# Kernel tuning notes

Measured on AMD Instinct MI355X. Metric: run time of the kernel, lower is better.

The kernel has to match this reference:

```python
import itertools
import jax, jax.numpy as jnp
import numpy as np

B, N, C, O = 8, 32, 64, 64
PERMS = list(itertools.permutations((1, 2, 3)))  # build_idx_3_permutations order


def _lin(k, fan_in, out, lead=()):
    # torch nn.Linear default init: U(-1/sqrt(fan_in), 1/sqrt(fan_in)) for W and b
    kw, kb = jax.random.split(k)
    bound = 1.0 / float(np.sqrt(fan_in))
    W = jax.random.uniform(kw, lead + (fan_in, out), minval=-bound, maxval=bound, dtype=jnp.float32)
    b = jax.random.uniform(kb, lead + (out,), minval=-bound, maxval=bound, dtype=jnp.float32)
    return W, b


def setup_inputs() -> dict:
    key = jax.random.key(0)
    ks = jax.random.split(key, 8)
    x = jax.random.normal(ks[0], (B, N, N, N, C), dtype=jnp.float32)
    W33, b33 = _lin(ks[1], 6 * C, O)            # three_to_three linear
    W22, b22 = _lin(ks[2], 12 * C, O, (3,))     # two_to_two (a2 cat transpose), 3 diagonal planes
    W12, b12 = _lin(ks[3], 10 * C, O, (3,))     # one_to_two
    W12t, b12t = _lin(ks[4], 10 * C, O, (3,))   # one_to_two_t
    W02, b02 = _lin(ks[5], 5 * C, O, (3,))      # zero_to_two
    W11, b11 = _lin(ks[6], 10 * C, O)           # one_to_one (in_node_channels = 0)
    W01, b01 = _lin(ks[7], 5 * C, O)            # zero_to_one
    return dict(x=x, W33=W33, b33=b33, W22=W22, b22=b22, W12=W12, b12=b12,
                W12t=W12t, b12t=b12t, W02=W02, b02=b02, W11=W11, b11=b11,
                W01=W01, b01=b01)


def _contractions(x):
    """All second/first/zeroth-order mean contractions of x: [B,n,n,n,C]."""
    s1, s2, s3 = x.mean(1), x.mean(2), x.mean(3)                      # [B,n,n,C]
    # diagonals arranged as [B, other_axis, diag_axis, C]
    d12 = jnp.moveaxis(jnp.diagonal(x, axis1=1, axis2=2), -1, 2)      # [B,n3,diag,C]
    d13 = jnp.moveaxis(jnp.diagonal(x, axis1=1, axis2=3), -1, 2)      # [B,n2,diag,C]
    d23 = jnp.moveaxis(jnp.diagonal(x, axis1=2, axis2=3), -1, 2)      # [B,n1,diag,C]
    a2 = jnp.concatenate([s1, s2, s3, d12, d13, d23], axis=-1)        # [B,n,n,6C]
    tdiag = jnp.moveaxis(jnp.diagonal(d23, axis1=1, axis2=2), -1, 1)  # [B,n,C] triple diagonal x[b,i,i,i]
    a1 = jnp.concatenate([
        x.mean((1, 2)), x.mean((1, 3)), x.mean((2, 3)),               # double sums
        d12.mean(1), d12.mean(2), d13.mean(1), d13.mean(2),           # diag sums
        d23.mean(1), d23.mean(2),
        tdiag], axis=-1)                                              # [B,n,10C]
    a0 = jnp.concatenate([
        x.mean((1, 2, 3)),                                            # triple sum
        d12.mean((1, 2)), d13.mean((1, 2)), d23.mean((1, 2)),         # diag-sum-sum
        tdiag.mean(1)], axis=-1)                                      # [B,5C]
    return a2, a1, a0


def reference(x, W33, b33, W22, b22, W12, b12, W12t, b12t, W02, b02, W11, b11, W01, b01):
    n = x.shape[1]
    a2, a1, a0 = _contractions(x)
    # third-order mix: concat all 6 spatial permutations, then linear 6C -> O
    allp = jnp.concatenate([jnp.transpose(x, (0,) + p + (4,)) for p in PERMS], axis=-1)
    T = allp @ W33 + b33                                              # [B,n,n,n,O]
    # second-order mixes for the 3 diagonal planes
    a2wt = jnp.concatenate([a2, jnp.swapaxes(a2, 1, 2)], axis=-1)     # [B,n,n,12C]
    slices = []
    for i in range(3):
        m = a2wt @ W22[i] + b22[i]
        m = m + (a1 @ W12[i] + b12[i])[:, :, None, :]
        m = m + (a1 @ W12t[i] + b12t[i])[:, None, :, :]
        m = m + (a0 @ W02[i] + b02[i])[:, None, None, :]
        slices.append(m)                                              # [B,n(other),n(diag),O]
    # first-order (core-diagonal) mix
    mdiag = a1 @ W11 + b11 + (a0 @ W01 + b01)[:, None, :]             # [B,n,O]
    # _expand_mix: accumulate slices onto diagonal planes of T (diagonal_free=False)
    idx = jnp.arange(n)
    # plane (1,2): T[b,d,d,t] += slices[0][b,t,d]
    T = T.at[:, idx, idx].add(jnp.swapaxes(slices[0], 1, 2))
    # plane (1,3): T[b,d,t,d] += slices[1][b,t,d]
    Tsw = jnp.swapaxes(T, 2, 3)
    Tsw = Tsw.at[:, idx, idx].add(jnp.swapaxes(slices[1], 1, 2))
    T = jnp.swapaxes(Tsw, 2, 3)
    # plane (2,3): T[b,t,d,d] += slices[2][b,t,d]
    T = T.at[:, :, idx, idx].add(slices[2])
    # triple diagonal: T[b,d,d,d] += mdiag[b,d]
    T = T.at[:, idx, idx, idx].add(mdiag)
    return T
```

## Files before the change

### kernel.cpp

```cpp
#include <hip/hip_runtime.h>

#define NBATCH 8
#define NN 32
#define NC 64
#define NO 64
#define C6 384
#define C10 640
#define C12 768
#define C5 320

typedef __attribute__((ext_vector_type(8))) short short8;
typedef __attribute__((ext_vector_type(4))) float float4v;

static constexpr int OFF_ABF = 0;
static constexpr int OFF_A1  = 1572864;
static constexpr int OFF_A0  = 1736704;
static constexpr int OFF_R1  = 1739264;
static constexpr int OFF_R1T = 1788416;
static constexpr int OFF_R0  = 1837568;
static constexpr int OFF_MD  = 1839104;
static constexpr int OFF_WB  = 1855488;
static constexpr int OFF_WB2 = 1867776;

__device__ __forceinline__ unsigned short f2bf(float f) {
    union { float f; unsigned u; } x{f};
    unsigned r = x.u + 0x7fffu + ((x.u >> 16) & 1u);
    return (unsigned short)(r >> 16);
}

__device__ __forceinline__ void store_bf4(unsigned short* p, float4v v) {
    ushort4 w;
    w.x = f2bf(v.x); w.y = f2bf(v.y); w.z = f2bf(v.z); w.w = f2bf(v.w);
    *(ushort4*)p = w;
}

__device__ __forceinline__ float4v bf4(const unsigned short* p) {
    ushort4 u = *(const ushort4*)(p);
    float4v r;
    r.x = __uint_as_float((unsigned)u.x << 16);
    r.y = __uint_as_float((unsigned)u.y << 16);
    r.z = __uint_as_float((unsigned)u.z << 16);
    r.w = __uint_as_float((unsigned)u.w << 16);
    return r;
}

__global__ __launch_bounds__(256) void k_prepw(const float* __restrict__ W33,
                                               const float* __restrict__ W22,
                                               float* __restrict__ ws) {
    int id = blockIdx.x * 256 + threadIdx.x;
    if (id < 3072) {
        int lane = id & 63;
        int ks = (id >> 6) % 12;
        int nt = (id >> 6) / 12;
        int n = nt * 16 + (lane & 15);
        int k0 = ks * 32 + (lane >> 4) * 8;
        unsigned short* dst = (unsigned short*)(ws + OFF_WB) +
                              (size_t)((nt * 12 + ks) * 64 + lane) * 8;
#pragma unroll
        for (int jj = 0; jj < 8; ++jj) dst[jj] = f2bf(W33[(k0 + jj) * 64 + n]);
    } else if (id < 21504) {
        int q = id - 3072;
        int lane = q & 63;
        int ks = (q >> 6) % 24;
        int r = (q >> 6) / 24;
        int nt = r & 3;
        int i = r >> 2;
        int n = nt * 16 + (lane & 15);
        int k0 = ks * 32 + (lane >> 4) * 8;
        const float* W = W22 + (size_t)i * C12 * NO;
        unsigned short* dst = (unsigned short*)(ws + OFF_WB2) +
                              (size_t)(((i * 4 + nt) * 24 + ks) * 64 + lane) * 8;
#pragma unroll
        for (int jj = 0; jj < 8; ++jj) dst[jj] = f2bf(W[(k0 + jj) * 64 + n]);
    }
}

__global__ __launch_bounds__(256) void k_contract2(const float* __restrict__ x,
                                                   float* __restrict__ ws) {
    int id = blockIdx.x * 256 + threadIdx.x;
    int c4 = id & 15;
    int v = (id >> 4) & 31;
    int u = (id >> 9) & 31;
    int b = id >> 14;
    int bc = c4 * 4;
    const float* xb = x + (size_t)b * 2097152;

    float4v s1 = {0.f, 0.f, 0.f, 0.f}, s2 = s1, s3 = s1;
    {
        const float* p = xb + u * 2048 + v * 64 + bc;
        for (int i = 0; i < 32; ++i) s1 += *(const float4v*)(p + i * 65536);
    }
    {
        const float* p = xb + u * 65536 + v * 64 + bc;
        for (int j = 0; j < 32; ++j) s2 += *(const float4v*)(p + j * 2048);
    }
    {
        const float* p = xb + u * 65536 + v * 2048 + bc;
        for (int k = 0; k < 32; ++k) s3 += *(const float4v*)(p + k * 64);
    }
    float4v d12 = *(const float4v*)(xb + v * 65536 + v * 2048 + u * 64 + bc);
    float4v d13 = *(const float4v*)(xb + v * 65536 + u * 2048 + v * 64 + bc);
    float4v d23 = *(const float4v*)(xb + u * 65536 + v * 2048 + v * 64 + bc);

    const float inv = 1.0f / 32.0f;
    unsigned short* a2 = (unsigned short*)(ws + OFF_ABF) +
                         (size_t)((b * 32 + u) * 32 + v) * C6 + bc;
    store_bf4(a2 + 0 * 64, s1 * inv);
    store_bf4(a2 + 1 * 64, s2 * inv);
    store_bf4(a2 + 2 * 64, s3 * inv);
    store_bf4(a2 + 3 * 64, d12);
    store_bf4(a2 + 4 * 64, d13);
    store_bf4(a2 + 5 * 64, d23);
}

__global__ __launch_bounds__(256) void k_contract1(const float* __restrict__ x,
                                                   float* __restrict__ ws) {
    int id = blockIdx.x * 256 + threadIdx.x;
    int c4 = id & 15;
    int t = (id >> 4) & 31;
    int b = id >> 9;
    int bc = c4 * 4;
    const unsigned short* a2 = (const unsigned short*)(ws + OFF_ABF) +
                               (size_t)b * 32 * 32 * C6;

    float4v su0 = {0.f,0.f,0.f,0.f}, su3 = su0, su4 = su0, su5 = su0;
    float4v sv0 = su0, sv1 = su0, sv3 = su0, sv4 = su0, sv5 = su0;
    for (int u = 0; u < 32; ++u) {
        const unsigned short* row = a2 + (size_t)(u * 32 + t) * C6 + bc;
        su0 += bf4(row + 0);
        su3 += bf4(row + 192);
        su4 += bf4(row + 256);
        su5 += bf4(row + 320);
    }
    for (int v = 0; v < 32; ++v) {
        const unsigned short* row = a2 + (size_t)(t * 32 + v) * C6 + bc;
        sv0 += bf4(row + 0);
        sv1 += bf4(row + 64);
        sv3 += bf4(row + 192);
        sv4 += bf4(row + 256);
        sv5 += bf4(row + 320);
    }
    float4v td = *(const float4v*)(x + (((size_t)b * 32 + t) * 32 + t) * 2048 + t * 64 + bc);

    float* a1 = ws + OFF_A1 + ((size_t)b * 32 + t) * C10;
    const float inv = 1.0f / 32.0f;
    *(float4v*)(a1 + 0 * 64 + bc) = su0 * inv;
    *(float4v*)(a1 + 1 * 64 + bc) = sv0 * inv;
    *(float4v*)(a1 + 2 * 64 + bc) = sv1 * inv;
    *(float4v*)(a1 + 3 * 64 + bc) = su3 * inv;
    *(float4v*)(a1 + 4 * 64 + bc) = sv3 * inv;
    *(float4v*)(a1 + 5 * 64 + bc) = su4 * inv;
    *(float4v*)(a1 + 6 * 64 + bc) = sv4 * inv;
    *(float4v*)(a1 + 7 * 64 + bc) = su5 * inv;
    *(float4v*)(a1 + 8 * 64 + bc) = sv5 * inv;
    *(float4v*)(a1 + 9 * 64 + bc) = td;
}

__global__ __launch_bounds__(256) void k_contract0(float* __restrict__ ws) {
    int id = blockIdx.x * 256 + threadIdx.x;
    if (id >= 512) return;
    int c = id & 63;
    int b = id >> 6;
    const float* a1 = ws + OFF_A1 + (size_t)b * 32 * C10;
    float s0 = 0, s1 = 0, s2 = 0, s3 = 0, s4 = 0;
    for (int t = 0; t < 32; ++t) {
        const float* row = a1 + t * C10;
        s0 += row[0 * 64 + c];
        s1 += row[3 * 64 + c];
        s2 += row[5 * 64 + c];
        s3 += row[7 * 64 + c];
        s4 += row[9 * 64 + c];
    }
    float* a0 = ws + OFF_A0 + b * C5;
    const float inv = 1.0f / 32.0f;
    a0[0 * 64 + c] = s0 * inv;
    a0[1 * 64 + c] = s1 * inv;
    a0[2 * 64 + c] = s2 * inv;
    a0[3 * 64 + c] = s3 * inv;
    a0[4 * 64 + c] = s4 * inv;
}

__global__ __launch_bounds__(256) void k_rowmix(
    const float* __restrict__ W12, const float* __restrict__ b12,
    const float* __restrict__ W12t, const float* __restrict__ b12t,
    const float* __restrict__ W02, const float* __restrict__ b02,
    const float* __restrict__ W11, const float* __restrict__ b11,
    const float* __restrict__ W01, const float* __restrict__ b01,
    float* __restrict__ ws) {
    int id = blockIdx.x * 256 + threadIdx.x;
    if (id < 98304) {
        bool second = id >= 49152;
        int q = second ? id - 49152 : id;
        int o = q & 63;
        int t = (q >> 6) & 31;
        int b = (q >> 11) & 7;
        int i = q >> 14;
        const float* W = (second ? W12t : W12) + (size_t)i * C10 * NO;
        const float* bb = (second ? b12t : b12) + i * NO;
        const float* a1 = ws + OFF_A1 + ((size_t)b * 32 + t) * C10;
        float acc = bb[o];
        for (int m = 0; m < C10; ++m) acc += a1[m] * W[m * NO + o];
        ws[(second ? OFF_R1T : OFF_R1) + (((size_t)i * 8 + b) * 32 + t) * NO + o] = acc;
    } else if (id < 114688) {
        int q = id - 98304;
        int o = q & 63;
        int t = (q >> 6) & 31;
        int b = q >> 11;
        const float* a1 = ws + OFF_A1 + ((size_t)b * 32 + t) * C10;
        const float* a0 = ws + OFF_A0 + (size_t)b * C5;
        float acc = b11[o] + b01[o];
        for (int m = 0; m < C10; ++m) acc += a1[m] * W11[m * NO + o];
        for (int m = 0; m < C5; ++m) acc += a0[m] * W01[m * NO + o];
        ws[OFF_MD + ((size_t)b * 32 + t) * NO + o] = acc;
    } else if (id < 116224) {
        int q = id - 114688;
        int o = q & 63;
        int b = (q >> 6) & 7;
        int i = q >> 9;
        const float* a0 = ws + OFF_A0 + (size_t)b * C5;
        float acc = b02[i * NO + o];
        for (int m = 0; m < C5; ++m) acc += a0[m] * W02[(size_t)i * C5 * NO + m * NO + o];
        ws[OFF_R0 + ((size_t)i * 8 + b) * NO + o] = acc;
    }
}

__global__ __launch_bounds__(256) void k_main(const float* __restrict__ x,
                                              const float* __restrict__ ws,
                                              const float* __restrict__ b33,
                                              float* __restrict__ T) {
    __shared__ __align__(16) unsigned short As[32 * 392];
    int tid = threadIdx.x;
    const unsigned short* WB = (const unsigned short*)(ws + OFF_WB);

    int wv = tid >> 6;
    int lane = tid & 63;
    int m_tile = wv & 1;
    int n_pair = wv >> 1;
    int colq = lane & 15;
    int quad = lane >> 4;

    short8 bfr[2][12];
#pragma unroll
    for (int np = 0; np < 2; ++np) {
        int nt = n_pair * 2 + np;
#pragma unroll
        for (int ks = 0; ks < 12; ++ks)
            bfr[np][ks] = *(const short8*)(WB + (size_t)((nt * 12 + ks) * 64 + lane) * 8);
    }
    float bb0 = b33[(n_pair * 2 + 0) * 16 + colq];
    float bb1 = b33[(n_pair * 2 + 1) * 16 + colq];

    int k0 = wv * 8;
    int c = colq * 4;
    int mrow = m_tile * 16 + colq;
    const unsigned short* Arow = &As[mrow * 392 + quad * 8];

    int tbase = (blockIdx.x & 7) * 1024 + (blockIdx.x >> 3) * 4;
#pragma unroll 1
    for (int r = 0; r < 4; ++r) {
        int tile = tbase + r;
        int b = tile >> 10;
        int i = (tile >> 5) & 31;
        int j = tile & 31;
        const float* xb = x + (size_t)b * 2097152;

#pragma unroll
        for (int half = 0; half < 2; ++half) {
            int k = k0 + quad + half * 4;
            float4v v0 = *(const float4v*)(xb + i * 65536 + j * 2048 + k * 64 + c);
            float4v v1 = *(const float4v*)(xb + i * 65536 + k * 2048 + j * 64 + c);
            float4v v2 = *(const float4v*)(xb + j * 65536 + i * 2048 + k * 64 + c);
            float4v v3 = *(const float4v*)(xb + k * 65536 + i * 2048 + j * 64 + c);
            float4v v4 = *(const float4v*)(xb + j * 65536 + k * 2048 + i * 64 + c);
            float4v v5 = *(const float4v*)(xb + k * 65536 + j * 2048 + i * 64 + c);
            unsigned short* dst = &As[k * 392 + c];
            store_bf4(dst + 0 * 64, v0);
            store_bf4(dst + 1 * 64, v1);
            store_bf4(dst + 2 * 64, v2);
            store_bf4(dst + 3 * 64, v3);
            store_bf4(dst + 4 * 64, v4);
            store_bf4(dst + 5 * 64, v5);
        }
        __syncthreads();

        float4v acc0 = {0.f, 0.f, 0.f, 0.f};
        float4v acc1 = {0.f, 0.f, 0.f, 0.f};
#pragma unroll
        for (int ks = 0; ks < 12; ++ks) {
            short8 a = *(const short8*)(Arow + ks * 32);
            acc0 = __builtin_amdgcn_mfma_f32_16x16x32_bf16(a, bfr[0][ks], acc0, 0, 0, 0);
            acc1 = __builtin_amdgcn_mfma_f32_16x16x32_bf16(a, bfr[1][ks], acc1, 0, 0, 0);
        }

        float* Tb = T + (size_t)tile * 2048;
#pragma unroll
        for (int rr = 0; rr < 4; ++rr) {
            int m = m_tile * 16 + quad * 4 + rr;
            int o0 = (n_pair * 2 + 0) * 16 + colq;
            int o1 = (n_pair * 2 + 1) * 16 + colq;
            __builtin_nontemporal_store(acc0[rr] + bb0, &Tb[m * 64 + o0]);
            __builtin_nontemporal_store(acc1[rr] + bb1, &Tb[m * 64 + o1]);
        }
        __syncthreads();
    }
}

__global__ __launch_bounds__(256) void k_slices(const float* __restrict__ b22,
                                                float* __restrict__ T,
                                                const float* __restrict__ ws) {
    __shared__ __align__(16) unsigned short As[32 * 776];
    int blk = blockIdx.x;
    int b = blk >> 5;
    int t = blk & 31;
    int tid = threadIdx.x;
    const unsigned short* abf = (const unsigned short*)(ws + OFF_ABF);
    const unsigned short* WB2 = (const unsigned short*)(ws + OFF_WB2);

    for (int l = tid; l < 3072; l += 256) {
        int d = l / 96;
        int m8 = l - d * 96;
        const unsigned short* src = (m8 < 48)
            ? abf + (size_t)(((b * 32 + t) * 32 + d) * C6) + m8 * 8
            : abf + (size_t)(((b * 32 + d) * 32 + t) * C6) + (m8 - 48) * 8;
        *(short8*)&As[d * 776 + m8 * 8] = *(const short8*)src;
    }
    __syncthreads();

    int wv = tid >> 6;
    int lane = tid & 63;
    int mt = wv & 1;
    int nh = wv >> 1;
    float4v zero = {0.f, 0.f, 0.f, 0.f};
    float4v acc[3][2] = {{zero, zero}, {zero, zero}, {zero, zero}};
    const unsigned short* Arow = &As[(mt * 16 + (lane & 15)) * 776 + (lane >> 4) * 8];
#pragma unroll
    for (int ks = 0; ks < 24; ++ks) {
        short8 a = *(const short8*)(Arow + ks * 32);
#pragma unroll
        for (int i = 0; i < 3; ++i) {
#pragma unroll
            for (int np = 0; np < 2; ++np) {
                int nt = nh * 2 + np;
                short8 bf = *(const short8*)(WB2 + (size_t)(((i * 4 + nt) * 24 + ks) * 64 + lane) * 8);
                acc[i][np] = __builtin_amdgcn_mfma_f32_16x16x32_bf16(a, bf, acc[i][np], 0, 0, 0);
            }
        }
    }

    int colq = lane & 15;
    int quad = lane >> 4;
    float* Tb = T + (size_t)b * 2097152;
#pragma unroll
    for (int np = 0; np < 2; ++np) {
        int o = (nh * 2 + np) * 16 + colq;
        float base0 = b22[0 * 64 + o] + ws[OFF_R1 + ((size_t)(0 * 8 + b) * 32 + t) * 64 + o]
                    + ws[OFF_R0 + (size_t)(0 * 8 + b) * 64 + o];
        float base1 = b22[1 * 64 + o] + ws[OFF_R1 + ((size_t)(1 * 8 + b) * 32 + t) * 64 + o]
                    + ws[OFF_R0 + (size_t)(1 * 8 + b) * 64 + o];
        float base2 = b22[2 * 64 + o] + ws[OFF_R1 + ((size_t)(2 * 8 + b) * 32 + t) * 64 + o]
                    + ws[OFF_R0 + (size_t)(2 * 8 + b) * 64 + o];
#pragma unroll
        for (int r = 0; r < 4; ++r) {
            int d = mt * 16 + quad * 4 + r;
            float s0 = acc[0][np][r] + base0 + ws[OFF_R1T + ((size_t)(0 * 8 + b) * 32 + d) * 64 + o];
            float s1 = acc[1][np][r] + base1 + ws[OFF_R1T + ((size_t)(1 * 8 + b) * 32 + d) * 64 + o];
            float s2 = acc[2][np][r] + base2 + ws[OFF_R1T + ((size_t)(2 * 8 + b) * 32 + d) * 64 + o];
            if (d != t) {
                Tb[d * 65536 + d * 2048 + t * 64 + o] += s0;
                Tb[d * 65536 + t * 2048 + d * 64 + o] += s1;
                Tb[t * 65536 + d * 2048 + d * 64 + o] += s2;
            } else {
                float md = ws[OFF_MD + ((size_t)b * 32 + d) * 64 + o];
                Tb[d * 65536 + d * 2048 + d * 64 + o] += s0 + s1 + s2 + md;
            }
        }
    }
}

extern "C" void kernel_launch(void* const* d_in, const int* in_sizes, int n_in,
                              void* d_out, int out_size, void* d_ws, size_t ws_size,
                              hipStream_t stream) {
    const float* x    = (const float*)d_in[0];
    const float* W33  = (const float*)d_in[1];
    const float* b33  = (const float*)d_in[2];
    const float* W22  = (const float*)d_in[3];
    const float* b22  = (const float*)d_in[4];
    const float* W12  = (const float*)d_in[5];
    const float* b12  = (const float*)d_in[6];
    const float* W12t = (const float*)d_in[7];
    const float* b12t = (const float*)d_in[8];
    const float* W02  = (const float*)d_in[9];
    const float* b02  = (const float*)d_in[10];
    const float* W11  = (const float*)d_in[11];
    const float* b11  = (const float*)d_in[12];
    const float* W01  = (const float*)d_in[13];
    const float* b01  = (const float*)d_in[14];
    float* T  = (float*)d_out;
    float* ws = (float*)d_ws;

    hipLaunchKernelGGL(k_prepw, dim3(84), dim3(256), 0, stream, W33, W22, ws);
    hipLaunchKernelGGL(k_contract2, dim3(512), dim3(256), 0, stream, x, ws);
    hipLaunchKernelGGL(k_contract1, dim3(16), dim3(256), 0, stream, x, ws);
    hipLaunchKernelGGL(k_contract0, dim3(2), dim3(256), 0, stream, ws);
    hipLaunchKernelGGL(k_rowmix, dim3(454), dim3(256), 0, stream,
                       W12, b12, W12t, b12t, W02, b02, W11, b11, W01, b01, ws);
    hipLaunchKernelGGL(k_main, dim3(2048), dim3(256), 0, stream, x, ws, b33, T);
    hipLaunchKernelGGL(k_slices, dim3(256), dim3(256), 0, stream, b22, T, ws);
}
```

Baseline: 277.0 us.

## Parallelize contract1 across blocks, fuse contract0 via atomics, widen k_slices

k_contract1 now runs one block per (batch, t) with a shared-memory tree reduction instead of 16 blocks of serial 32-step loops. The old k_contract0 kernel is folded in through atomicAdd into a0, which is zeroed with a memset beforehand. k_slices moves to 512 threads so each wave owns one N-tile instead of two, giving more waves per block. The goal is to remove tiny low-occupancy launches from the critical path. The cost is float atomics with nondeterministic summation order and an extra memset on the stream.

New measurement: 250.4 us. 9.6% less time.

```diff
diff --git a/kernel.cpp b/kernel.cpp
--- a/kernel.cpp
+++ b/kernel.cpp
@@ -115,69 +115,72 @@
 
 __global__ __launch_bounds__(256) void k_contract1(const float* __restrict__ x,
                                                    float* __restrict__ ws) {
-    int id = blockIdx.x * 256 + threadIdx.x;
-    int c4 = id & 15;
-    int t = (id >> 4) & 31;
-    int b = id >> 9;
+    __shared__ float4v red[16][148];
+    int blk = blockIdx.x;
+    int b = blk >> 5;
+    int t = blk & 31;
+    int tid = threadIdx.x;
+    int c4 = tid & 15;
+    int q = tid >> 4;
     int bc = c4 * 4;
     const unsigned short* a2 = (const unsigned short*)(ws + OFF_ABF) +
                                (size_t)b * 32 * 32 * C6;
 
-    float4v su0 = {0.f,0.f,0.f,0.f}, su3 = su0, su4 = su0, su5 = su0;
-    float4v sv0 = su0, sv1 = su0, sv3 = su0, sv4 = su0, sv5 = su0;
-    for (int u = 0; u < 32; ++u) {
-        const unsigned short* row = a2 + (size_t)(u * 32 + t) * C6 + bc;
-        su0 += bf4(row + 0);
-        su3 += bf4(row + 192);
-        su4 += bf4(row + 256);
-        su5 += bf4(row + 320);
-    }
-    for (int v = 0; v < 32; ++v) {
-        const unsigned short* row = a2 + (size_t)(t * 32 + v) * C6 + bc;
-        sv0 += bf4(row + 0);
-        sv1 += bf4(row + 64);
-        sv3 += bf4(row + 192);
-        sv4 += bf4(row + 256);
-        sv5 += bf4(row + 320);
-    }
-    float4v td = *(const float4v*)(x + (((size_t)b * 32 + t) * 32 + t) * 2048 + t * 64 + bc);
-
+    float4v pu0 = {0.f, 0.f, 0.f, 0.f};
+    float4v pu3 = pu0, pu4 = pu0, pu5 = pu0;
+    float4v pv0 = pu0, pv1 = pu0, pv3 = pu0, pv4 = pu0, pv5 = pu0;
+#pragma unroll
+    for (int s = 0; s < 2; ++s) {
+        int u = q * 2 + s;
+        const unsigned short* rU = a2 + (size_t)(u * 32 + t) * C6 + bc;
+        const unsigned short* rV = a2 + (size_t)(t * 32 + u) * C6 + bc;
+        pu0 += bf4(rU + 0);
+        pu3 += bf4(rU + 192);
+        pu4 += bf4(rU + 256);
+        pu5 += bf4(rU + 320);
+        pv0 += bf4(rV + 0);
+        pv1 += bf4(rV + 64);
+        pv3 += bf4(rV + 192);
+        pv4 += bf4(rV + 256);
+        pv5 += bf4(rV + 320);
+    }
+    red[q][0 * 16 + c4] = pu0;
+    red[q][1 * 16 + c4] = pv0;
+    red[q][2 * 16 + c4] = pv1;
+    red[q][3 * 16 + c4] = pu3;
+    red[q][4 * 16 + c4] = pv3;
+    red[q][5 * 16 + c4] = pu4;
+    red[q][6 * 16 + c4] = pv4;
+    red[q][7 * 16 + c4] = pu5;
+    red[q][8 * 16 + c4] = pv5;
+    __syncthreads();
+
+    const float inv = 1.0f / 32.0f;
     float* a1 = ws + OFF_A1 + ((size_t)b * 32 + t) * C10;
-    const float inv = 1.0f / 32.0f;
-    *(float4v*)(a1 + 0 * 64 + bc) = su0 * inv;
-    *(float4v*)(a1 + 1 * 64 + bc) = sv0 * inv;
-    *(float4v*)(a1 + 2 * 64 + bc) = sv1 * inv;
-    *(float4v*)(a1 + 3 * 64 + bc) = su3 * inv;
-    *(float4v*)(a1 + 4 * 64 + bc) = sv3 * inv;
-    *(float4v*)(a1 + 5 * 64 + bc) = su4 * inv;
-    *(float4v*)(a1 + 6 * 64 + bc) = sv4 * inv;
-    *(float4v*)(a1 + 7 * 64 + bc) = su5 * inv;
-    *(float4v*)(a1 + 8 * 64 + bc) = sv5 * inv;
-    *(float4v*)(a1 + 9 * 64 + bc) = td;
-}
-
-__global__ __launch_bounds__(256) void k_contract0(float* __restrict__ ws) {
-    int id = blockIdx.x * 256 + threadIdx.x;
-    if (id >= 512) return;
-    int c = id & 63;
-    int b = id >> 6;
-    const float* a1 = ws + OFF_A1 + (size_t)b * 32 * C10;
-    float s0 = 0, s1 = 0, s2 = 0, s3 = 0, s4 = 0;
-    for (int t = 0; t < 32; ++t) {
-        const float* row = a1 + t * C10;
-        s0 += row[0 * 64 + c];
-        s1 += row[3 * 64 + c];
-        s2 += row[5 * 64 + c];
-        s3 += row[7 * 64 + c];
-        s4 += row[9 * 64 + c];
-    }
-    float* a0 = ws + OFF_A0 + b * C5;
-    const float inv = 1.0f / 32.0f;
-    a0[0 * 64 + c] = s0 * inv;
-    a0[1 * 64 + c] = s1 * inv;
-    a0[2 * 64 + c] = s2 * inv;
-    a0[3 * 64 + c] = s3 * inv;
-    a0[4 * 64 + c] = s4 * inv;
+    float* a0 = ws + OFF_A0 + (size_t)b * C5;
+    if (tid < 144) {
+        int ch = tid >> 4;
+        int cc = tid & 15;
+        float4v s = {0.f, 0.f, 0.f, 0.f};
+#pragma unroll
+        for (int qq = 0; qq < 16; ++qq) s += red[qq][ch * 16 + cc];
+        s *= inv;
+        *(float4v*)(a1 + ch * 64 + cc * 4) = s;
+        int aidx = (ch == 0) ? 0 : (ch == 3) ? 1 : (ch == 5) ? 2 : (ch == 7) ? 3 : -1;
+        if (aidx >= 0) {
+#pragma unroll
+            for (int e = 0; e < 4; ++e)
+                atomicAdd(a0 + aidx * 64 + cc * 4 + e, s[e] * inv);
+        }
+    } else if (tid < 160) {
+        int cc = tid - 144;
+        float4v td = *(const float4v*)(x + (((size_t)b * 32 + t) * 32 + t) * 2048 +
+                                       t * 64 + cc * 4);
+        *(float4v*)(a1 + 9 * 64 + cc * 4) = td;
+#pragma unroll
+        for (int e = 0; e < 4; ++e)
+            atomicAdd(a0 + 4 * 64 + cc * 4 + e, td[e] * inv);
+    }
 }
 
 __global__ __launch_bounds__(256) void k_rowmix(
@@ -305,7 +308,7 @@
     }
 }
 
-__global__ __launch_bounds__(256) void k_slices(const float* __restrict__ b22,
+__global__ __launch_bounds__(512) void k_slices(const float* __restrict__ b22,
                                                 float* __restrict__ T,
                                                 const float* __restrict__ ws) {
     __shared__ __align__(16) unsigned short As[32 * 776];
@@ -316,7 +319,7 @@
     const unsigned short* abf = (const unsigned short*)(ws + OFF_ABF);
     const unsigned short* WB2 = (const unsigned short*)(ws + OFF_WB2);
 
-    for (int l = tid; l < 3072; l += 256) {
+    for (int l = tid; l < 3072; l += 512) {
         int d = l / 96;
         int m8 = l - d * 96;
         const unsigned short* src = (m8 < 48)
@@ -329,50 +332,43 @@
     int wv = tid >> 6;
     int lane = tid & 63;
     int mt = wv & 1;
-    int nh = wv >> 1;
+    int nt = wv >> 1;
     float4v zero = {0.f, 0.f, 0.f, 0.f};
-    float4v acc[3][2] = {{zero, zero}, {zero, zero}, {zero, zero}};
+    float4v acc[3] = {zero, zero, zero};
     const unsigned short* Arow = &As[(mt * 16 + (lane & 15)) * 776 + (lane >> 4) * 8];
 #pragma unroll
     for (int ks = 0; ks < 24; ++ks) {
         short8 a = *(const short8*)(Arow + ks * 32);
 #pragma unroll
         for (int i = 0; i < 3; ++i) {
-#pragma unroll
-            for (int np = 0; np < 2; ++np) {
-                int nt = nh * 2 + np;
-                short8 bf = *(const short8*)(WB2 + (size_t)(((i * 4 + nt) * 24 + ks) * 64 + lane) * 8);
-                acc[i][np] = __builtin_amdgcn_mfma_f32_16x16x32_bf16(a, bf, acc[i][np], 0, 0, 0);
-            }
+            short8 bf = *(const short8*)(WB2 + (size_t)(((i * 4 + nt) * 24 + ks) * 64 + lane) * 8);
+            acc[i] = __builtin_amdgcn_mfma_f32_16x16x32_bf16(a, bf, acc[i], 0, 0, 0);
         }
     }
 
     int colq = lane & 15;
     int quad = lane >> 4;
     float* Tb = T + (size_t)b * 2097152;
-#pragma unroll
-    for (int np = 0; np < 2; ++np) {
-        int o = (nh * 2 + np) * 16 + colq;
-        float base0 = b22[0 * 64 + o] + ws[OFF_R1 + ((size_t)(0 * 8 + b) * 32 + t) * 64 + o]
-                    + ws[OFF_R0 + (size_t)(0 * 8 + b) * 64 + o];
-        float base1 = b22[1 * 64 + o] + ws[OFF_R1 + ((size_t)(1 * 8 + b) * 32 + t) * 64 + o]
-                    + ws[OFF_R0 + (size_t)(1 * 8 + b) * 64 + o];
-        float base2 = b22[2 * 64 + o] + ws[OFF_R1 + ((size_t)(2 * 8 + b) * 32 + t) * 64 + o]
-                    + ws[OFF_R0 + (size_t)(2 * 8 + b) * 64 + o];
-#pragma unroll
-        for (int r = 0; r < 4; ++r) {
-            int d = mt * 16 + quad * 4 + r;
-            float s0 = acc[0][np][r] + base0 + ws[OFF_R1T + ((size_t)(0 * 8 + b) * 32 + d) * 64 + o];
-            float s1 = acc[1][np][r] + base1 + ws[OFF_R1T + ((size_t)(1 * 8 + b) * 32 + d) * 64 + o];
-            float s2 = acc[2][np][r] + base2 + ws[OFF_R1T + ((size_t)(2 * 8 + b) * 32 + d) * 64 + o];
-            if (d != t) {
-                Tb[d * 65536 + d * 2048 + t * 64 + o] += s0;
-                Tb[d * 65536 + t * 2048 + d * 64 + o] += s1;
-                Tb[t * 65536 + d * 2048 + d * 64 + o] += s2;
-            } else {
-                float md = ws[OFF_MD + ((size_t)b * 32 + d) * 64 + o];
-                Tb[d * 65536 + d * 2048 + d * 64 + o] += s0 + s1 + s2 + md;
-            }
+    int o = nt * 16 + colq;
+    float base0 = b22[0 * 64 + o] + ws[OFF_R1 + ((size_t)(0 * 8 + b) * 32 + t) * 64 + o]
+                + ws[OFF_R0 + (size_t)(0 * 8 + b) * 64 + o];
+    float base1 = b22[1 * 64 + o] + ws[OFF_R1 + ((size_t)(1 * 8 + b) * 32 + t) * 64 + o]
+                + ws[OFF_R0 + (size_t)(1 * 8 + b) * 64 + o];
+    float base2 = b22[2 * 64 + o] + ws[OFF_R1 + ((size_t)(2 * 8 + b) * 32 + t) * 64 + o]
+                + ws[OFF_R0 + (size_t)(2 * 8 + b) * 64 + o];
+#pragma unroll
+    for (int r = 0; r < 4; ++r) {
+        int d = mt * 16 + quad * 4 + r;
+        float s0 = acc[0][r] + base0 + ws[OFF_R1T + ((size_t)(0 * 8 + b) * 32 + d) * 64 + o];
+        float s1 = acc[1][r] + base1 + ws[OFF_R1T + ((size_t)(1 * 8 + b) * 32 + d) * 64 + o];
+        float s2 = acc[2][r] + base2 + ws[OFF_R1T + ((size_t)(2 * 8 + b) * 32 + d) * 64 + o];
+        if (d != t) {
+            Tb[d * 65536 + d * 2048 + t * 64 + o] += s0;
+            Tb[d * 65536 + t * 2048 + d * 64 + o] += s1;
+            Tb[t * 65536 + d * 2048 + d * 64 + o] += s2;
+        } else {
+            float md = ws[OFF_MD + ((size_t)b * 32 + d) * 64 + o];
+            Tb[d * 65536 + d * 2048 + d * 64 + o] += s0 + s1 + s2 + md;
         }
     }
 }
@@ -400,10 +396,10 @@
 
     hipLaunchKernelGGL(k_prepw, dim3(84), dim3(256), 0, stream, W33, W22, ws);
     hipLaunchKernelGGL(k_contract2, dim3(512), dim3(256), 0, stream, x, ws);
-    hipLaunchKernelGGL(k_contract1, dim3(16), dim3(256), 0, stream, x, ws);
-    hipLaunchKernelGGL(k_contract0, dim3(2), dim3(256), 0, stream, ws);
+    hipMemsetAsync(ws + OFF_A0, 0, (size_t)NBATCH * C5 * sizeof(float), stream);
+    hipLaunchKernelGGL(k_contract1, dim3(256), dim3(256), 0, stream, x, ws);
     hipLaunchKernelGGL(k_rowmix, dim3(454), dim3(256), 0, stream,
                        W12, b12, W12t, b12t, W02, b02, W11, b11, W01, b01, ws);
     hipLaunchKernelGGL(k_main, dim3(2048), dim3(256), 0, stream, x, ws, b33, T);
-    hipLaunchKernelGGL(k_slices, dim3(256), dim3(256), 0, stream, b22, T, ws);
-}
+    hipLaunchKernelGGL(k_slices, dim3(256), dim3(512), 0, stream, b22, T, ws);
+}
```
